# Performance work log

Measured on AMD Instinct MI355X. Metric: run time of the kernel, lower is better.

Reference implementation:

```python
import jax, jax.numpy as jnp
import numpy as np

EPS = 1e-6
NUM_HEADS = 16


def _layernorm(x, g, b):
    m = jnp.mean(x, axis=-1, keepdims=True)
    v = jnp.mean(jnp.square(x - m), axis=-1, keepdims=True)
    return (x - m) * jax.lax.rsqrt(v + EPS) * g + b


def setup_inputs() -> dict:
    key = jax.random.key(0)
    ks = jax.random.split(key, 16)
    B, Lq, Lkv, D = 2, 2048, 4096, 2048
    Hd = D // NUM_HEADS
    s = 0.02
    return {
        "hidden_states": jax.random.normal(ks[0], (B, Lq, D), jnp.float32),
        "cross_attention_states": jax.random.normal(ks[1], (B, Lkv, D), jnp.float32),
        "q_w": jax.random.normal(ks[2], (D, D), jnp.float32) * s,
        "q_b": jnp.zeros((D,), jnp.float32),
        "k_w": jax.random.normal(ks[3], (D, D), jnp.float32) * s,
        "k_b": jnp.zeros((D,), jnp.float32),
        "v_w": jax.random.normal(ks[4], (D, D), jnp.float32) * s,
        "v_b": jnp.zeros((D,), jnp.float32),
        "o_w": jax.random.normal(ks[5], (D, D), jnp.float32) * s,
        "o_b": jnp.zeros((D,), jnp.float32),
        "qn_g": jnp.ones((Hd,), jnp.float32),
        "qn_b": jnp.zeros((Hd,), jnp.float32),
        "kn_g": jnp.ones((Hd,), jnp.float32),
        "kn_b": jnp.zeros((Hd,), jnp.float32),
    }


def reference(hidden_states, cross_attention_states,
              q_w, q_b, k_w, k_b, v_w, v_b, o_w, o_b,
              qn_g, qn_b, kn_g, kn_b):
    B, Lq, D = hidden_states.shape
    H = NUM_HEADS
    Hd = D // H
    scale = Hd ** -0.5

    # torch Linear: y = x @ W^T + b
    q = hidden_states @ q_w.T + q_b                        # [B,Lq,D]
    k = cross_attention_states @ k_w.T + k_b               # [B,Lkv,D]
    v = cross_attention_states @ v_w.T + v_b               # [B,Lkv,D]

    q = q.reshape(B, Lq, H, Hd).transpose(0, 2, 1, 3)      # [B,H,Lq,Hd]
    k = k.reshape(B, -1, H, Hd).transpose(0, 2, 1, 3)      # [B,H,Lkv,Hd]
    v = v.reshape(B, -1, H, Hd).transpose(0, 2, 1, 3)      # [B,H,Lkv,Hd]

    # per-head QK LayerNorm before scores
    q = _layernorm(q, qn_g, qn_b)
    k = _layernorm(k, kn_g, kn_b)

    attn_weights = jnp.einsum('bhqd,bhkd->bhqk', q, k) * scale
    attn_weights = jax.nn.softmax(attn_weights.astype(jnp.float32), axis=-1).astype(q.dtype)
    # dropout p=0.0 (inference) -> identity

    attn_output = jnp.einsum('bhqk,bhkd->bhqd', attn_weights, v)
    attn_output = attn_output.transpose(0, 2, 1, 3).reshape(B, Lq, D)
    attn_output = attn_output @ o_w.T + o_b
    return attn_output, attn_weights
```

## Files before the change

### kernel.cpp

```cpp
#include <hip/hip_runtime.h>
#include <cstdint>
#include <cstddef>

using u16 = unsigned short;
using f32x4 = __attribute__((ext_vector_type(4))) float;
using bf8   = __attribute__((ext_vector_type(8))) short;

#define DEVFN __device__ __forceinline__

constexpr int BB  = 2;
constexpr int LQ  = 2048;
constexpr int LKV = 4096;
constexpr int DD  = 2048;
constexpr int NH  = 16;
constexpr int HDm = 128;
constexpr float ATTN_SCALE = 0.08838834764831845f;
constexpr float LN_EPS = 1e-6f;
constexpr float LOG2E  = 1.4426950408889634f;
constexpr float SHIFT2 = 17.312340490667562f;

DEVFN u16 f2bf(float f) {
  unsigned u = __builtin_bit_cast(unsigned, f);
  u += 0x7fffu + ((u >> 16) & 1u);
  return (u16)(u >> 16);
}
DEVFN float bf2f(u16 h) { return __builtin_bit_cast(float, (unsigned)h << 16); }
DEVFN f32x4 mfma16(bf8 a, bf8 b, f32x4 c) {
  return __builtin_amdgcn_mfma_f32_16x16x32_bf16(a, b, c, 0, 0, 0);
}
DEVFN void gl16(const void* g, void* l) {
  __builtin_amdgcn_global_load_lds(
      (const __attribute__((address_space(1))) void*)g,
      (__attribute__((address_space(3))) void*)l, 16, 0, 0);
}
DEVFN void barrier_hard() {
  __builtin_amdgcn_s_barrier();
  __builtin_amdgcn_sched_barrier(0);
}

__global__ __launch_bounds__(256) void k_cvt(const float4* __restrict__ in,
                                             ushort4* __restrict__ out, int n4) {
  int i = blockIdx.x * 256 + threadIdx.x;
  if (i >= n4) return;
  float4 v = in[i];
  ushort4 o;
  o.x = f2bf(v.x); o.y = f2bf(v.y); o.z = f2bf(v.z); o.w = f2bf(v.w);
  out[i] = o;
}

template <int MODE>
__global__ __launch_bounds__(256) void k_gemm_nt(const u16* __restrict__ X,
                                                 const u16* __restrict__ Wt,
                                                 const float* __restrict__ bias,
                                                 const float* __restrict__ lng,
                                                 const float* __restrict__ lnb,
                                                 void* __restrict__ Y,
                                                 int M, int N, int K) {
  __shared__ __align__(16) u16 Sh[2][128 * 64];
  __shared__ float Sm[2][128], Sq[2][128];
  u16* As = Sh[0];
  u16* Bs = Sh[1];
  const int tid = threadIdx.x;
  const int w = tid >> 6, l = tid & 63;
  const int m0 = blockIdx.x * 128, n0 = blockIdx.y * 128;
  const int wr = w >> 1, wc = w & 1;
  const int lr = l & 15, lk = (l >> 4) * 8;
  const int rsw = (l & 7) << 3;
  const int srow = l >> 3;
  const int scb = (l & 7) * 16;
  f32x4 acc[4][4] = {};

  for (int k0 = 0; k0 < K; k0 += 64) {
#pragma unroll
    for (int i = 0; i < 4; ++i) {
      int rbase = w * 32 + i * 8;
      int row = rbase + srow;
      int cb = scb ^ ((row & 7) << 4);
      gl16((const char*)&X[(size_t)(m0 + row) * K + k0] + cb, &As[rbase * 64]);
      gl16((const char*)&Wt[(size_t)(n0 + row) * K + k0] + cb, &Bs[rbase * 64]);
    }
    __syncthreads();
    bf8 af[4][2], bfr[4][2];
#pragma unroll
    for (int mi = 0; mi < 4; ++mi)
#pragma unroll
      for (int kk = 0; kk < 2; ++kk)
        af[mi][kk] = *(const bf8*)&As[(wr * 64 + mi * 16 + lr) * 64 + ((kk * 32 + lk) ^ rsw)];
#pragma unroll
    for (int ni = 0; ni < 4; ++ni)
#pragma unroll
      for (int kk = 0; kk < 2; ++kk)
        bfr[ni][kk] = *(const bf8*)&Bs[(wc * 64 + ni * 16 + lr) * 64 + ((kk * 32 + lk) ^ rsw)];
#pragma unroll
    for (int kk = 0; kk < 2; ++kk)
#pragma unroll
      for (int mi = 0; mi < 4; ++mi)
#pragma unroll
        for (int ni = 0; ni < 4; ++ni)
          acc[mi][ni] = mfma16(af[mi][kk], bfr[ni][kk], acc[mi][ni]);
    __syncthreads();
  }
  const int lrg = (l >> 4) * 4;

  float bv[4];
#pragma unroll
  for (int ni = 0; ni < 4; ++ni) bv[ni] = bias[n0 + wc * 64 + ni * 16 + lr];
#pragma unroll
  for (int mi = 0; mi < 4; ++mi)
#pragma unroll
    for (int ni = 0; ni < 4; ++ni)
#pragma unroll
      for (int r = 0; r < 4; ++r) acc[mi][ni][r] += bv[ni];

  if constexpr (MODE == 2 || MODE == 3) {
#pragma unroll
    for (int mi = 0; mi < 4; ++mi) {
#pragma unroll
      for (int r = 0; r < 4; ++r) {
        float ps = 0.f, pq = 0.f;
#pragma unroll
        for (int ni = 0; ni < 4; ++ni) {
          float v = acc[mi][ni][r];
          ps += v; pq += v * v;
        }
#pragma unroll
        for (int m = 1; m < 16; m <<= 1) {
          ps += __shfl_xor(ps, m);
          pq += __shfl_xor(pq, m);
        }
        if (lr == 0) {
          int rl = wr * 64 + mi * 16 + lrg + r;
          Sm[wc][rl] = ps; Sq[wc][rl] = pq;
        }
      }
    }
    __syncthreads();
    float gv[4], bbv[4];
#pragma unroll
    for (int ni = 0; ni < 4; ++ni) {
      int c = wc * 64 + ni * 16 + lr;
      gv[ni] = lng[c]; bbv[ni] = lnb[c];
    }
#pragma unroll
    for (int mi = 0; mi < 4; ++mi)
#pragma unroll
      for (int r = 0; r < 4; ++r) {
        int rl = wr * 64 + mi * 16 + lrg + r;
        float mean = (Sm[0][rl] + Sm[1][rl]) * (1.f / 128.f);
        float var  = (Sq[0][rl] + Sq[1][rl]) * (1.f / 128.f) - mean * mean;
        float rs = rsqrtf(var + LN_EPS);
#pragma unroll
        for (int ni = 0; ni < 4; ++ni) {
          float o = (acc[mi][ni][r] - mean) * rs * gv[ni] + bbv[ni];
          if (MODE == 3) o *= ATTN_SCALE;
          acc[mi][ni][r] = o;
        }
      }
  }

  if constexpr (MODE == 4) {
    u16* T = &Sh[0][0];
#pragma unroll
    for (int mi = 0; mi < 4; ++mi)
#pragma unroll
      for (int ni = 0; ni < 4; ++ni)
#pragma unroll
        for (int r = 0; r < 4; ++r) {
          int mrow = wr * 64 + mi * 16 + lrg + r;
          int ncol = wc * 64 + ni * 16 + lr;
          T[mrow * 128 + (ncol ^ ((mrow & 7) << 3))] = f2bf(acc[mi][ni][r]);
        }
    __syncthreads();
    int hd = tid >> 1, half = tid & 1;
    int bq = m0 >> 12;
    int kvb = (m0 & (LKV - 1)) + half * 64;
    int hh = n0 >> 7;
    u16* vout = (u16*)Y + ((size_t)(bq * NH + hh) * HDm + hd) * LKV + kvb;
#pragma unroll
    for (int j8 = 0; j8 < 8; ++j8) {
      u16 tmp[8] __attribute__((aligned(16)));
#pragma unroll
      for (int j = 0; j < 8; ++j) {
        int kv = half * 64 + j8 * 8 + j;
        tmp[j] = T[kv * 128 + (hd ^ ((kv & 7) << 3))];
      }
      *(int4*)&vout[j8 * 8] = *(const int4*)tmp;
    }
    return;
  }

#pragma unroll
  for (int ni = 0; ni < 4; ++ni) {
    int n = n0 + wc * 64 + ni * 16 + lr;
#pragma unroll
    for (int mi = 0; mi < 4; ++mi) {
      int mb = m0 + wr * 64 + mi * 16 + lrg;
#pragma unroll
      for (int r = 0; r < 4; ++r) {
        float v = acc[mi][ni][r];
        if constexpr (MODE == 1)
          __builtin_nontemporal_store(v, &((float*)Y)[(size_t)(mb + r) * N + n]);
        else
          ((u16*)Y)[(size_t)(mb + r) * N + n] = f2bf(v);
      }
    }
  }
}

__global__ __launch_bounds__(512, 4) void k_attn(const u16* __restrict__ Qp,
                                                 const u16* __restrict__ Kp,
                                                 const u16* __restrict__ Vt,
                                                 float* __restrict__ Wout,
                                                 u16* __restrict__ AO) {
  const int g = blockIdx.x;
  const int work = (g & 7) * 64 + (g >> 3);
  const int bh = work >> 4;
  const int b = bh >> 4, h = bh & 15;
  const int q0 = (work & 15) * 128;
  const int tid = threadIdx.x, w = tid >> 6, l = tid & 63;
  const int lr = l & 15, lk = (l >> 4) * 8, lrg = (l >> 4) * 4;
  const int rsw = (l & 7) << 3;
  __shared__ __align__(16) u16 Ks[2][64 * 128];
  __shared__ __align__(16) u16 Vs[2][128 * 64];
  __shared__ __align__(16) u16 Ps[8][16 * 64];

  bf8 qf[4];
  {
    const u16* qb = &Qp[((size_t)b * LQ + q0 + w * 16 + lr) * DD + h * HDm];
#pragma unroll
    for (int kc = 0; kc < 4; ++kc) qf[kc] = *(const bf8*)(qb + kc * 32 + lk);
  }
  const u16* Kb = Kp + (size_t)b * LKV * DD + h * HDm;
  const u16* Vb = Vt + (size_t)bh * HDm * LKV;

  auto stageK = [&](int buf, int kv0) {
#pragma unroll
    for (int i = 0; i < 2; ++i) {
      int rbase = i * 32 + w * 4;
      int row = rbase + (l >> 4);
      int cb = ((l & 15) * 16) ^ ((row & 7) << 4);
      gl16((const char*)(Kb + (size_t)(kv0 + row) * DD) + cb, &Ks[buf][rbase * 128]);
    }
  };
  auto stageV = [&](int buf, int kv0) {
#pragma unroll
    for (int i = 0; i < 2; ++i) {
      int rbase = i * 64 + w * 8;
      int row = rbase + (l >> 3);
      int cb = ((l & 7) * 16) ^ ((row & 7) << 4);
      gl16((const char*)(Vb + (size_t)row * LKV + kv0) + cb, &Vs[buf][rbase * 64]);
    }
  };
  auto qk_tile = [&](int t, f32x4 (&s)[4]) {
    const u16* ks = Ks[t & 1];
    __builtin_amdgcn_s_setprio(1);
#pragma unroll
    for (int ni = 0; ni < 4; ++ni) {
      s[ni] = f32x4{0.f, 0.f, 0.f, 0.f};
#pragma unroll
      for (int kc = 0; kc < 4; ++kc) {
        bf8 kf = *(const bf8*)&ks[(ni * 16 + lr) * 128 + ((kc * 32 + lk) ^ rsw)];
        s[ni] = mfma16(qf[kc], kf, s[ni]);
      }
    }
    __builtin_amdgcn_s_setprio(0);
  };

  float lsum[4] = {0.f, 0.f, 0.f, 0.f};
  auto sumexp = [&](const f32x4 (&s)[4]) {
#pragma unroll
    for (int ni = 0; ni < 4; ++ni)
#pragma unroll
      for (int r = 0; r < 4; ++r)
        lsum[r] += exp2f(fmaf(s[ni][r], LOG2E, -SHIFT2));
  };
  f32x4 sA[4], sB[4];
  stageK(0, 0);
  asm volatile("s_waitcnt vmcnt(0)" ::: "memory");
  barrier_hard();
  stageK(1, 64);
  qk_tile(0, sA);
  asm volatile("s_waitcnt vmcnt(0)" ::: "memory");
  barrier_hard();
  for (int t = 1; t < 64; t += 2) {
    if (t < 63) stageK((t + 1) & 1, (t + 1) * 64);
    qk_tile(t, sB);
    sumexp(sA);
    asm volatile("s_waitcnt vmcnt(0)" ::: "memory");
    barrier_hard();
    if (t + 1 < 64) {
      if (t + 1 < 63) stageK((t + 2) & 1, (t + 2) * 64);
      qk_tile(t + 1, sA);
      sumexp(sB);
      asm volatile("s_waitcnt vmcnt(0)" ::: "memory");
      barrier_hard();
    }
  }
  sumexp(sB);
  float cr[4];
#pragma unroll
  for (int r = 0; r < 4; ++r) {
    float v = lsum[r];
#pragma unroll
    for (int m = 1; m < 16; m <<= 1) v += __shfl_xor(v, m);
    cr[r] = -(SHIFT2 + __log2f(v));
  }

  f32x4 oacc[8] = {};
  float* wbase = Wout + ((size_t)bh * LQ + q0 + w * 16 + lrg) * LKV;
  auto finish = [&](int tp, const f32x4 (&s)[4]) {
    const int kv0 = tp * 64;
#pragma unroll
    for (int ni = 0; ni < 4; ++ni) {
#pragma unroll
      for (int r = 0; r < 4; ++r) {
        float p = exp2f(fmaf(s[ni][r], LOG2E, cr[r]));
        __builtin_nontemporal_store(p, &wbase[(size_t)r * LKV + kv0 + ni * 16 + lr]);
        int row = lrg + r;
        Ps[w][row * 64 + ((ni * 16 + lr) ^ ((row & 7) << 3))] = f2bf(p);
      }
    }
    asm volatile("s_waitcnt lgkmcnt(0)" ::: "memory");
    __builtin_amdgcn_sched_barrier(0);
    __builtin_amdgcn_s_setprio(1);
#pragma unroll
    for (int kk = 0; kk < 2; ++kk) {
      bf8 pf = *(const bf8*)&Ps[w][lr * 64 + ((kk * 32 + lk) ^ rsw)];
#pragma unroll
      for (int c = 0; c < 8; ++c) {
        bf8 vf = *(const bf8*)&Vs[tp & 1][(c * 16 + lr) * 64 + ((kk * 32 + lk) ^ rsw)];
        oacc[c] = mfma16(pf, vf, oacc[c]);
      }
    }
    __builtin_amdgcn_s_setprio(0);
  };

  stageK(0, 0);
  asm volatile("s_waitcnt vmcnt(0)" ::: "memory");
  barrier_hard();
  stageK(1, 64); stageV(0, 0);
  qk_tile(0, sA);
  asm volatile("s_waitcnt vmcnt(0)" ::: "memory");
  barrier_hard();
  for (int t = 1; t < 64; t += 2) {
    if (t < 63) stageK((t + 1) & 1, (t + 1) * 64);
    stageV(t & 1, t * 64);
    qk_tile(t, sB);
    finish(t - 1, sA);
    asm volatile("s_waitcnt vmcnt(16)" ::: "memory");
    barrier_hard();
    if (t + 1 < 64) {
      if (t + 1 < 63) stageK((t + 2) & 1, (t + 2) * 64);
      stageV((t + 1) & 1, (t + 1) * 64);
      qk_tile(t + 1, sA);
      finish(t, sB);
      asm volatile("s_waitcnt vmcnt(16)" ::: "memory");
      barrier_hard();
    }
  }
  finish(63, sB);

#pragma unroll
  for (int c = 0; c < 8; ++c)
#pragma unroll
    for (int r = 0; r < 4; ++r)
      AO[((size_t)b * LQ + q0 + w * 16 + lrg + r) * DD + h * HDm + c * 16 + lr] =
          f2bf(oacc[c][r]);
}

extern "C" void kernel_launch(void* const* d_in, const int* in_sizes, int n_in,
                              void* d_out, int out_size, void* d_ws, size_t ws_size,
                              hipStream_t stream) {
  const float* hs   = (const float*)d_in[0];
  const float* cas  = (const float*)d_in[1];
  const float* q_w  = (const float*)d_in[2];
  const float* q_b  = (const float*)d_in[3];
  const float* k_w  = (const float*)d_in[4];
  const float* k_b  = (const float*)d_in[5];
  const float* v_w  = (const float*)d_in[6];
  const float* v_b  = (const float*)d_in[7];
  const float* o_w  = (const float*)d_in[8];
  const float* o_b  = (const float*)d_in[9];
  const float* qn_g = (const float*)d_in[10];
  const float* qn_b = (const float*)d_in[11];
  const float* kn_g = (const float*)d_in[12];
  const float* kn_b = (const float*)d_in[13];

  float* out_attn = (float*)d_out;
  float* out_w    = out_attn + (size_t)BB * LQ * DD;

  constexpr size_t SZ_Q  = (size_t)BB * LQ * DD * 2;
  constexpr size_t SZ_KV = (size_t)BB * LKV * DD * 2;
  constexpr size_t SZ_W  = (size_t)DD * DD * 2;
  char* p = (char*)d_ws;
  u16* hsb  = (u16*)p;              p += SZ_Q;
  u16* casb = (u16*)p;              p += SZ_KV;
  u16* qwb  = (u16*)p;              p += SZ_W;
  u16* kwb  = (u16*)p;              p += SZ_W;
  u16* vwb  = (u16*)p;              p += SZ_W;
  u16* owb  = (u16*)p;              p += SZ_W;
  u16* Qp   = (u16*)p;              p += SZ_Q;
  u16* Kp   = (u16*)p;              p += SZ_KV;
  u16* Vtp  = (u16*)p;              p += SZ_KV;
  u16* AO   = (u16*)p;              p += SZ_Q;

  auto cvt = [&](const float* src, u16* dst, size_t n) {
    int n4 = (int)(n / 4);
    k_cvt<<<dim3((n4 + 255) / 256), dim3(256), 0, stream>>>(
        (const float4*)src, (ushort4*)dst, n4);
  };
  cvt(hs,  hsb,  (size_t)BB * LQ * DD);
  cvt(cas, casb, (size_t)BB * LKV * DD);
  cvt(q_w, qwb, (size_t)DD * DD);
  cvt(k_w, kwb, (size_t)DD * DD);
  cvt(v_w, vwb, (size_t)DD * DD);
  cvt(o_w, owb, (size_t)DD * DD);

  k_gemm_nt<3><<<dim3(BB * LQ / 128, DD / 128), dim3(256), 0, stream>>>(
      hsb, qwb, q_b, qn_g, qn_b, Qp, BB * LQ, DD, DD);
  k_gemm_nt<2><<<dim3(BB * LKV / 128, DD / 128), dim3(256), 0, stream>>>(
      casb, kwb, k_b, kn_g, kn_b, Kp, BB * LKV, DD, DD);
  k_gemm_nt<4><<<dim3(BB * LKV / 128, DD / 128), dim3(256), 0, stream>>>(
      casb, vwb, v_b, nullptr, nullptr, Vtp, BB * LKV, DD, DD);

  k_attn<<<dim3(LQ / 128 * BB * NH), dim3(512), 0, stream>>>(Qp, Kp, Vtp, out_w, AO);

  k_gemm_nt<1><<<dim3(BB * LQ / 128, DD / 128), dim3(256), 0, stream>>>(
      AO, owb, o_b, nullptr, nullptr, out_attn, BB * LQ, DD, DD);
}
```

Before: 790.0 us.

## Transpose score MFMA to vectorize weight stores and replace LDS P staging with shuffles

```diff
diff --git a/kernel.cpp b/kernel.cpp
--- a/kernel.cpp
+++ b/kernel.cpp
@@ -5,6 +5,7 @@
 using u16 = unsigned short;
 using f32x4 = __attribute__((ext_vector_type(4))) float;
 using bf8   = __attribute__((ext_vector_type(8))) short;
+using u32x4 = __attribute__((ext_vector_type(4))) unsigned;
 
 #define DEVFN __device__ __forceinline__
 
@@ -218,11 +219,11 @@
   const int b = bh >> 4, h = bh & 15;
   const int q0 = (work & 15) * 128;
   const int tid = threadIdx.x, w = tid >> 6, l = tid & 63;
-  const int lr = l & 15, lk = (l >> 4) * 8, lrg = (l >> 4) * 4;
+  const int lr = l & 15, lk = (l >> 4) * 8;
+  const int gq = l >> 4;
   const int rsw = (l & 7) << 3;
   __shared__ __align__(16) u16 Ks[2][64 * 128];
   __shared__ __align__(16) u16 Vs[2][128 * 64];
-  __shared__ __align__(16) u16 Ps[8][16 * 64];
 
   bf8 qf[4];
   {
@@ -233,6 +234,15 @@
   const u16* Kb = Kp + (size_t)b * LKV * DD + h * HDm;
   const u16* Vb = Vt + (size_t)bh * HDm * LKV;
 
+  auto stageK128 = [&](u16* buf, int kv0) {
+#pragma unroll
+    for (int i = 0; i < 4; ++i) {
+      int rbase = i * 32 + w * 4;
+      int row = rbase + (l >> 4);
+      int cb = ((l & 15) * 16) ^ ((row & 7) << 4);
+      gl16((const char*)(Kb + (size_t)(kv0 + row) * DD) + cb, &buf[rbase * 128]);
+    }
+  };
   auto stageK = [&](int buf, int kv0) {
 #pragma unroll
     for (int i = 0; i < 2; ++i) {
@@ -251,120 +261,102 @@
       gl16((const char*)(Vb + (size_t)row * LKV + kv0) + cb, &Vs[buf][rbase * 64]);
     }
   };
-  auto qk_tile = [&](int t, f32x4 (&s)[4]) {
-    const u16* ks = Ks[t & 1];
+
+  u16* bufA0 = &Ks[0][0];
+  u16* bufA1 = &Vs[0][0];
+  float lsum = 0.f;
+  stageK128(bufA0, 0);
+  asm volatile("s_waitcnt vmcnt(0)" ::: "memory");
+  barrier_hard();
+  for (int t = 0; t < 32; ++t) {
+    const u16* kb = (t & 1) ? bufA1 : bufA0;
+    if (t < 31) stageK128((t & 1) ? bufA0 : bufA1, (t + 1) * 128);
+    f32x4 s8[8];
+    __builtin_amdgcn_s_setprio(1);
+#pragma unroll
+    for (int ni = 0; ni < 8; ++ni) {
+      s8[ni] = f32x4{0.f, 0.f, 0.f, 0.f};
+#pragma unroll
+      for (int kc = 0; kc < 4; ++kc) {
+        bf8 kf = *(const bf8*)&kb[(ni * 16 + lr) * 128 + ((kc * 32 + lk) ^ rsw)];
+        s8[ni] = mfma16(kf, qf[kc], s8[ni]);
+      }
+    }
+    __builtin_amdgcn_s_setprio(0);
+#pragma unroll
+    for (int ni = 0; ni < 8; ++ni)
+#pragma unroll
+      for (int r = 0; r < 4; ++r)
+        lsum += exp2f(fmaf(s8[ni][r], LOG2E, -SHIFT2));
+    asm volatile("s_waitcnt vmcnt(0)" ::: "memory");
+    barrier_hard();
+  }
+  lsum += __shfl_xor(lsum, 16);
+  lsum += __shfl_xor(lsum, 32);
+  const float cr = -(SHIFT2 + __log2f(lsum));
+
+  f32x4 oacc[8] = {};
+  float* wq = Wout + ((size_t)bh * LQ + q0 + w * 16 + lr) * LKV;
+  const int srcA = lr + ((gq & 1) << 5);
+  const int srcB = srcA + 16;
+  const bool hi = (gq >> 1) != 0;
+
+  stageK(0, 0); stageV(0, 0);
+  asm volatile("s_waitcnt vmcnt(0)" ::: "memory");
+  barrier_hard();
+  for (int t = 0; t < 64; ++t) {
+    const int cur = t & 1;
+    const int kv0 = t * 64;
+    if (t < 63) { stageK(cur ^ 1, kv0 + 64); stageV(cur ^ 1, kv0 + 64); }
+    f32x4 s[4];
     __builtin_amdgcn_s_setprio(1);
 #pragma unroll
     for (int ni = 0; ni < 4; ++ni) {
       s[ni] = f32x4{0.f, 0.f, 0.f, 0.f};
 #pragma unroll
       for (int kc = 0; kc < 4; ++kc) {
-        bf8 kf = *(const bf8*)&ks[(ni * 16 + lr) * 128 + ((kc * 32 + lk) ^ rsw)];
-        s[ni] = mfma16(qf[kc], kf, s[ni]);
+        bf8 kf = *(const bf8*)&Ks[cur][(ni * 16 + lr) * 128 + ((kc * 32 + lk) ^ rsw)];
+        s[ni] = mfma16(kf, qf[kc], s[ni]);
       }
     }
     __builtin_amdgcn_s_setprio(0);
-  };
-
-  float lsum[4] = {0.f, 0.f, 0.f, 0.f};
-  auto sumexp = [&](const f32x4 (&s)[4]) {
-#pragma unroll
-    for (int ni = 0; ni < 4; ++ni)
-#pragma unroll
-      for (int r = 0; r < 4; ++r)
-        lsum[r] += exp2f(fmaf(s[ni][r], LOG2E, -SHIFT2));
-  };
-  f32x4 sA[4], sB[4];
-  stageK(0, 0);
-  asm volatile("s_waitcnt vmcnt(0)" ::: "memory");
-  barrier_hard();
-  stageK(1, 64);
-  qk_tile(0, sA);
-  asm volatile("s_waitcnt vmcnt(0)" ::: "memory");
-  barrier_hard();
-  for (int t = 1; t < 64; t += 2) {
-    if (t < 63) stageK((t + 1) & 1, (t + 1) * 64);
-    qk_tile(t, sB);
-    sumexp(sA);
-    asm volatile("s_waitcnt vmcnt(0)" ::: "memory");
+    unsigned pk2[4][2];
+#pragma unroll
+    for (int ni = 0; ni < 4; ++ni) {
+      float p0 = exp2f(fmaf(s[ni][0], LOG2E, cr));
+      float p1 = exp2f(fmaf(s[ni][1], LOG2E, cr));
+      float p2 = exp2f(fmaf(s[ni][2], LOG2E, cr));
+      float p3 = exp2f(fmaf(s[ni][3], LOG2E, cr));
+      f32x4 pv4 = {p0, p1, p2, p3};
+      __builtin_nontemporal_store(pv4, (f32x4*)(wq + kv0 + ni * 16 + 4 * gq));
+      pk2[ni][0] = (unsigned)f2bf(p0) | ((unsigned)f2bf(p1) << 16);
+      pk2[ni][1] = (unsigned)f2bf(p2) | ((unsigned)f2bf(p3) << 16);
+    }
+#pragma unroll
+    for (int kk = 0; kk < 2; ++kk) {
+      unsigned xa0 = __shfl(pk2[2 * kk][0], srcA), xa1 = __shfl(pk2[2 * kk][1], srcA);
+      unsigned ya0 = __shfl(pk2[2 * kk + 1][0], srcA), ya1 = __shfl(pk2[2 * kk + 1][1], srcA);
+      unsigned xb0 = __shfl(pk2[2 * kk][0], srcB), xb1 = __shfl(pk2[2 * kk][1], srcB);
+      unsigned yb0 = __shfl(pk2[2 * kk + 1][0], srcB), yb1 = __shfl(pk2[2 * kk + 1][1], srcB);
+      u32x4 pf32 = { hi ? ya0 : xa0, hi ? ya1 : xa1, hi ? yb0 : xb0, hi ? yb1 : xb1 };
+      bf8 pf = __builtin_bit_cast(bf8, pf32);
+      __builtin_amdgcn_s_setprio(1);
+#pragma unroll
+      for (int c = 0; c < 8; ++c) {
+        bf8 vf = *(const bf8*)&Vs[cur][(c * 16 + lr) * 64 + ((kk * 32 + lk) ^ rsw)];
+        oacc[c] = mfma16(pf, vf, oacc[c]);
+      }
+      __builtin_amdgcn_s_setprio(0);
+    }
+    asm volatile("s_waitcnt vmcnt(4)" ::: "memory");
     barrier_hard();
-    if (t + 1 < 64) {
-      if (t + 1 < 63) stageK((t + 2) & 1, (t + 2) * 64);
-      qk_tile(t + 1, sA);
-      sumexp(sB);
-      asm volatile("s_waitcnt vmcnt(0)" ::: "memory");
-      barrier_hard();
-    }
-  }
-  sumexp(sB);
-  float cr[4];
-#pragma unroll
-  for (int r = 0; r < 4; ++r) {
-    float v = lsum[r];
-#pragma unroll
-    for (int m = 1; m < 16; m <<= 1) v += __shfl_xor(v, m);
-    cr[r] = -(SHIFT2 + __log2f(v));
-  }
-
-  f32x4 oacc[8] = {};
-  float* wbase = Wout + ((size_t)bh * LQ + q0 + w * 16 + lrg) * LKV;
-  auto finish = [&](int tp, const f32x4 (&s)[4]) {
-    const int kv0 = tp * 64;
-#pragma unroll
-    for (int ni = 0; ni < 4; ++ni) {
-#pragma unroll
-      for (int r = 0; r < 4; ++r) {
-        float p = exp2f(fmaf(s[ni][r], LOG2E, cr[r]));
-        __builtin_nontemporal_store(p, &wbase[(size_t)r * LKV + kv0 + ni * 16 + lr]);
-        int row = lrg + r;
-        Ps[w][row * 64 + ((ni * 16 + lr) ^ ((row & 7) << 3))] = f2bf(p);
-      }
-    }
-    asm volatile("s_waitcnt lgkmcnt(0)" ::: "memory");
-    __builtin_amdgcn_sched_barrier(0);
-    __builtin_amdgcn_s_setprio(1);
-#pragma unroll
-    for (int kk = 0; kk < 2; ++kk) {
-      bf8 pf = *(const bf8*)&Ps[w][lr * 64 + ((kk * 32 + lk) ^ rsw)];
-#pragma unroll
-      for (int c = 0; c < 8; ++c) {
-        bf8 vf = *(const bf8*)&Vs[tp & 1][(c * 16 + lr) * 64 + ((kk * 32 + lk) ^ rsw)];
-        oacc[c] = mfma16(pf, vf, oacc[c]);
-      }
-    }
-    __builtin_amdgcn_s_setprio(0);
-  };
-
-  stageK(0, 0);
-  asm volatile("s_waitcnt vmcnt(0)" ::: "memory");
-  barrier_hard();
-  stageK(1, 64); stageV(0, 0);
-  qk_tile(0, sA);
-  asm volatile("s_waitcnt vmcnt(0)" ::: "memory");
-  barrier_hard();
-  for (int t = 1; t < 64; t += 2) {
-    if (t < 63) stageK((t + 1) & 1, (t + 1) * 64);
-    stageV(t & 1, t * 64);
-    qk_tile(t, sB);
-    finish(t - 1, sA);
-    asm volatile("s_waitcnt vmcnt(16)" ::: "memory");
-    barrier_hard();
-    if (t + 1 < 64) {
-      if (t + 1 < 63) stageK((t + 2) & 1, (t + 2) * 64);
-      stageV((t + 1) & 1, (t + 1) * 64);
-      qk_tile(t + 1, sA);
-      finish(t, sB);
-      asm volatile("s_waitcnt vmcnt(16)" ::: "memory");
-      barrier_hard();
-    }
-  }
-  finish(63, sB);
+  }
 
 #pragma unroll
   for (int c = 0; c < 8; ++c)
 #pragma unroll
     for (int r = 0; r < 4; ++r)
-      AO[((size_t)b * LQ + q0 + w * 16 + lrg + r) * DD + h * HDm + c * 16 + lr] =
+      AO[((size_t)b * LQ + q0 + w * 16 + 4 * gq + r) * DD + h * HDm + c * 16 + lr] =
           f2bf(oacc[c][r]);
 }
 
```

Measured after the change: 753.5 us. -4.6%, faster.
